# Optimization experiments

Hardware: AMD Instinct MI355X
Metric: run time of the kernel (lower is better)

The kernel has to match this reference:

```python
import jax, jax.numpy as jnp
import numpy as np
import math

D_KEY = 64
D_VALUE = 64
NUM_HEADS = 16
D_MODEL = D_VALUE * NUM_HEADS  # 1024


def setup_inputs() -> dict:
    key = jax.random.key(0)
    ks = jax.random.split(key, 5)
    B, N = 2, 2048
    s = 1.0 / math.sqrt(D_MODEL)
    return {
        "x": jax.random.normal(ks[0], (B, N, D_MODEL), dtype=jnp.float32),
        "Wq": jax.random.normal(ks[1], (D_MODEL, D_KEY * NUM_HEADS), dtype=jnp.float32) * s,
        "Wk": jax.random.normal(ks[2], (D_MODEL, D_KEY * NUM_HEADS), dtype=jnp.float32) * s,
        "Wv": jax.random.normal(ks[3], (D_MODEL, D_MODEL), dtype=jnp.float32) * s,
        "Wp": jax.random.normal(ks[4], (D_MODEL, D_MODEL), dtype=jnp.float32) * s,
    }


def reference(x, Wq, Wk, Wv, Wp):
    # x: [B, N, d_model]. Equivalent to the original block-diagonal concat trick:
    # off-diagonal blocks are -inf, so softmax over the key axis reduces to
    # independent per-head softmax attention.
    B, N, D = x.shape
    H, K, V = NUM_HEADS, D_KEY, D_VALUE
    scale = 1.0 / math.sqrt(K)
    q = (x @ Wq).reshape(B, N, H, K)
    k = (x @ Wk).reshape(B, N, H, K)
    v = (x @ Wv).reshape(B, N, H, V)
    scores = jnp.einsum("bnhk,bmhk->bhnm", q, k) * scale  # [B,H,N,N]
    attn = jax.nn.softmax(scores, axis=-1)
    out = jnp.einsum("bhnm,bmhv->bnhv", attn, v).reshape(B, N, D)
    return x + out @ Wp
```

## Files before the change

kernel.cpp:

```cpp
#include <hip/hip_runtime.h>

typedef float f32x4 __attribute__((ext_vector_type(4)));
typedef __bf16 bf16x8 __attribute__((ext_vector_type(8)));

#define DEV static __device__ __forceinline__

DEV ushort f2bf(float f) {
  unsigned u = __builtin_bit_cast(unsigned, f);
  u += 0x7FFFu + ((u >> 16) & 1u);
  return (ushort)(u >> 16);
}

DEV bf16x8 ld_frag(const ushort* p) {
  return __builtin_bit_cast(bf16x8, *reinterpret_cast<const int4*>(p));
}

DEV bf16x8 ld_lds(const ushort* base, int byte_off) {
  return __builtin_bit_cast(bf16x8,
      *reinterpret_cast<const int4*>(reinterpret_cast<const char*>(base) + byte_off));
}

DEV int swz(int row, int col_byte) { return row * 128 + (col_byte ^ ((row & 7) << 4)); }

DEV float fast_exp2(float x) {
  float r;
  asm("v_exp_f32 %0, %1" : "=v"(r) : "v"(x));
  return r;
}

DEV unsigned cvt_pk_bf16(float lo, float hi) {
  unsigned r;
  asm("v_cvt_pk_bf16_f32 %0, %1, %2" : "=v"(r) : "v"(lo), "v"(hi));
  return r;
}

DEV void gload16(const ushort* g, ushort* l) {
  __builtin_amdgcn_global_load_lds(
      (const __attribute__((address_space(1))) unsigned int*)g,
      (__attribute__((address_space(3))) unsigned int*)l, 16, 0, 0);
}


__global__ __launch_bounds__(256) void convert_x(const float* __restrict__ x,
                                                 ushort* __restrict__ xb) {
  int i = blockIdx.x * 256 + threadIdx.x;
  float4 v = reinterpret_cast<const float4*>(x)[i];
  ushort4 o = make_ushort4(f2bf(v.x), f2bf(v.y), f2bf(v.z), f2bf(v.w));
  reinterpret_cast<ushort4*>(xb)[i] = o;
}

__global__ __launch_bounds__(256) void transpose_w(const float* __restrict__ w0,
                                                   const float* __restrict__ w1,
                                                   const float* __restrict__ w2,
                                                   const float* __restrict__ w3,
                                                   ushort* __restrict__ wt) {
  __shared__ float tile[32][33];
  const int z = blockIdx.z;
  const float* w = z == 0 ? w0 : z == 1 ? w1 : z == 2 ? w2 : w3;
  ushort* out = wt + (size_t)z * 1024 * 1024;
  const int n0 = blockIdx.x * 32, k0 = blockIdx.y * 32;
  const int tx = threadIdx.x, ty = threadIdx.y;
#pragma unroll
  for (int i = 0; i < 4; ++i)
    tile[ty + i * 8][tx] = w[(size_t)(k0 + ty + i * 8) * 1024 + n0 + tx];
  __syncthreads();
#pragma unroll
  for (int i = 0; i < 4; ++i)
    out[(size_t)(n0 + ty + i * 8) * 1024 + k0 + tx] = f2bf(tile[tx][ty + i * 8]);
}


DEV void gemm_core(const ushort* __restrict__ A, const ushort* __restrict__ BT,
                   ushort* a_lds, ushort* b_lds, int row0, int col0, f32x4 acc[4][4]) {
  const int tid = threadIdx.x;
  const int lane = tid & 63;
  const int w = tid >> 6, wr = w >> 1, wc = w & 1;
  const int lg = lane >> 4, l15 = lane & 15;
  const int srow = w * 32 + (lane >> 3);
  const int scol = ((lane & 7) ^ (lane >> 3)) << 3;
  const ushort* ga = A + (size_t)(row0 + srow) * 1024 + scol;
  const ushort* gb = BT + (size_t)(col0 + srow) * 1024 + scol;
#pragma unroll
  for (int ai = 0; ai < 4; ++ai)
#pragma unroll
    for (int bj = 0; bj < 4; ++bj) acc[ai][bj] = f32x4{0.f, 0.f, 0.f, 0.f};

  for (int kt = 0; kt < 1024; kt += 64) {
    __syncthreads();
#pragma unroll
    for (int p = 0; p < 4; ++p) {
      gload16(ga + kt + (size_t)(p * 8) * 1024, a_lds + (w * 32 + p * 8) * 64);
      gload16(gb + kt + (size_t)(p * 8) * 1024, b_lds + (w * 32 + p * 8) * 64);
    }
    __syncthreads();
    bf16x8 af[4][2], bfr[4][2];
#pragma unroll
    for (int i = 0; i < 4; ++i)
#pragma unroll
      for (int kk = 0; kk < 2; ++kk) {
        af[i][kk] = ld_lds(a_lds, swz(wr * 64 + i * 16 + l15, kk * 64 + lg * 16));
        bfr[i][kk] = ld_lds(b_lds, swz(wc * 64 + i * 16 + l15, kk * 64 + lg * 16));
      }
#pragma unroll
    for (int kk = 0; kk < 2; ++kk)
#pragma unroll
      for (int ai = 0; ai < 4; ++ai)
#pragma unroll
        for (int bj = 0; bj < 4; ++bj)
          acc[ai][bj] = __builtin_amdgcn_mfma_f32_16x16x32_bf16(af[ai][kk], bfr[bj][kk],
                                                                acc[ai][bj], 0, 0, 0);
  }
}

__global__ __launch_bounds__(256) void gemm_qkv(const ushort* __restrict__ xb,
                                                const ushort* __restrict__ wqT,
                                                const ushort* __restrict__ wkT,
                                                const ushort* __restrict__ wvT,
                                                ushort* __restrict__ q, ushort* __restrict__ k,
                                                ushort* __restrict__ vt) {
  __shared__ ushort a_lds[128 * 64], b_lds[128 * 64];
  const int fid = blockIdx.x;
  const int wid = (fid & 7) * 96 + (fid >> 3);
  const int row = wid / 24, rem = wid % 24;
  const int col = rem / 3, z = rem % 3;
  const int row0 = row * 128, col0 = col * 128;
  const ushort* BT = z == 0 ? wqT : z == 1 ? wkT : wvT;
  f32x4 acc[4][4];
  gemm_core(xb, BT, a_lds, b_lds, row0, col0, acc);
  const int lane = threadIdx.x & 63;
  const int w = threadIdx.x >> 6, wr = w >> 1, wc = w & 1;
  const int lg = lane >> 4, l15 = lane & 15;
  if (z < 2) {
    ushort* out = z == 0 ? q : k;
    const float sc = z == 0 ? 0.125f * 1.4426950408889634f : 1.0f;
#pragma unroll
    for (int ai = 0; ai < 4; ++ai)
#pragma unroll
      for (int bj = 0; bj < 4; ++bj)
#pragma unroll
        for (int r = 0; r < 4; ++r) {
          int orow = row0 + wr * 64 + ai * 16 + lg * 4 + r;
          int ocol = col0 + wc * 64 + bj * 16 + l15;
          out[(size_t)orow * 1024 + ocol] = f2bf(acc[ai][bj][r] * sc);
        }
  } else {
#pragma unroll
    for (int ai = 0; ai < 4; ++ai)
#pragma unroll
      for (int bj = 0; bj < 4; ++bj) {
        int orow = row0 + wr * 64 + ai * 16 + lg * 4;
        int ocol = col0 + wc * 64 + bj * 16 + l15;
        int bb = orow >> 11, n = orow & 2047;
        ushort4 pk = make_ushort4(f2bf(acc[ai][bj][0]), f2bf(acc[ai][bj][1]),
                                  f2bf(acc[ai][bj][2]), f2bf(acc[ai][bj][3]));
        *reinterpret_cast<ushort4*>(vt + ((size_t)(bb * 1024 + ocol)) * 2048 + n) = pk;
      }
  }
}

__global__ __launch_bounds__(256) void gemm_out(const ushort* __restrict__ ob,
                                                const ushort* __restrict__ wpT,
                                                const float* __restrict__ x,
                                                float* __restrict__ y) {
  __shared__ ushort a_lds[128 * 64], b_lds[64 * 64];
  const int fid = blockIdx.x;
  const int wid = (fid & 7) * 64 + (fid >> 3);
  const int row0 = (wid >> 4) * 128, col0 = (wid & 15) * 64;
  const int tid = threadIdx.x;
  const int lane = tid & 63;
  const int w = tid >> 6, wr = w >> 1, wc = w & 1;
  const int lg = lane >> 4, l15 = lane & 15;
  const int sr8 = lane >> 3;
  const int scol = ((lane & 7) ^ sr8) << 3;
  const ushort* ga = ob + (size_t)(row0 + w * 32 + sr8) * 1024 + scol;
  const ushort* gb = wpT + (size_t)(col0 + w * 16 + sr8) * 1024 + scol;

  f32x4 acc[4][2];
#pragma unroll
  for (int ai = 0; ai < 4; ++ai)
#pragma unroll
    for (int bj = 0; bj < 2; ++bj) acc[ai][bj] = f32x4{0.f, 0.f, 0.f, 0.f};

  for (int kt = 0; kt < 1024; kt += 64) {
    __syncthreads();
#pragma unroll
    for (int p = 0; p < 4; ++p)
      gload16(ga + kt + (size_t)(p * 8) * 1024, a_lds + (w * 32 + p * 8) * 64);
#pragma unroll
    for (int p = 0; p < 2; ++p)
      gload16(gb + kt + (size_t)(p * 8) * 1024, b_lds + (w * 16 + p * 8) * 64);
    __syncthreads();
    bf16x8 af[4][2], bfr[2][2];
#pragma unroll
    for (int kk = 0; kk < 2; ++kk) {
#pragma unroll
      for (int i = 0; i < 4; ++i)
        af[i][kk] = ld_lds(a_lds, swz(wr * 64 + i * 16 + l15, kk * 64 + lg * 16));
#pragma unroll
      for (int j = 0; j < 2; ++j)
        bfr[j][kk] = ld_lds(b_lds, swz(wc * 32 + j * 16 + l15, kk * 64 + lg * 16));
    }
#pragma unroll
    for (int kk = 0; kk < 2; ++kk)
#pragma unroll
      for (int ai = 0; ai < 4; ++ai)
#pragma unroll
        for (int bj = 0; bj < 2; ++bj)
          acc[ai][bj] = __builtin_amdgcn_mfma_f32_16x16x32_bf16(af[ai][kk], bfr[bj][kk],
                                                                acc[ai][bj], 0, 0, 0);
  }

#pragma unroll
  for (int ai = 0; ai < 4; ++ai)
#pragma unroll
    for (int bj = 0; bj < 2; ++bj)
#pragma unroll
      for (int r = 0; r < 4; ++r) {
        int orow = row0 + wr * 64 + ai * 16 + lg * 4 + r;
        int ocol = col0 + wc * 32 + bj * 16 + l15;
        size_t idx = (size_t)orow * 1024 + ocol;
        y[idx] = x[idx] + acc[ai][bj][r];
      }
}

__global__ __launch_bounds__(256) void attn(const ushort* __restrict__ qg,
                                            const ushort* __restrict__ kg,
                                            const ushort* __restrict__ vtg,
                                            ushort* __restrict__ og) {
  __shared__ ushort k_lds[2 * 64 * 64];
  __shared__ ushort v_lds[2 * 64 * 64];
  const int fid = blockIdx.x;
  const int wid = (fid & 7) * 128 + (fid >> 3);
  const int bh = wid >> 5, q0 = wid & 31;
  const int b = bh >> 4, h = bh & 15;
  const int n0 = q0 * 64;
  const int tid = threadIdx.x, lane = tid & 63, w = tid >> 6;
  const int lg = lane >> 4, l15 = lane & 15;

  bf16x8 qf[2];
#pragma unroll
  for (int d32 = 0; d32 < 2; ++d32)
    qf[d32] = ld_frag(qg + (size_t)(b * 2048 + n0 + w * 16 + l15) * 1024 + h * 64 + d32 * 32 + lg * 8);

  f32x4 o[4];
#pragma unroll
  for (int bj = 0; bj < 4; ++bj) o[bj] = f32x4{0.f, 0.f, 0.f, 0.f};
  f32x4 ssum = f32x4{0.f, 0.f, 0.f, 0.f};

  const int sr8 = lane >> 3;
  const int scol = ((lane & 7) ^ sr8) << 3;
  const ushort* kbase = kg + (size_t)(b * 2048 + w * 16 + sr8) * 1024 + h * 64 + scol;
  const ushort* vbase = vtg + (size_t)(b * 1024 + h * 64 + w * 16 + sr8) * 2048 + scol;

  ushort* kB0 = k_lds;
  ushort* kB1 = k_lds + 4096;
  ushort* vB0 = v_lds;
  ushort* vB1 = v_lds + 4096;

  auto stage = [&](ushort* kdst, ushort* vdst, int kv0) {
#pragma unroll
    for (int p = 0; p < 2; ++p) {
      gload16(kbase + (size_t)(kv0 + p * 8) * 1024, kdst + (w * 16 + p * 8) * 64);
      gload16(vbase + (size_t)(p * 8) * 2048 + kv0, vdst + (w * 16 + p * 8) * 64);
    }
  };

  const int4 ones4 = make_int4(0x3F803F80, 0x3F803F80, 0x3F803F80, 0x3F803F80);
  const bf16x8 onesf = __builtin_bit_cast(bf16x8, ones4);

  auto body = [&](const ushort* kb, const ushort* vb) {
    f32x4 s[4];
#pragma unroll
    for (int kj = 0; kj < 4; ++kj) s[kj] = f32x4{0.f, 0.f, 0.f, 0.f};
    __builtin_amdgcn_s_setprio(1);
#pragma unroll
    for (int d32 = 0; d32 < 2; ++d32)
#pragma unroll
      for (int kj = 0; kj < 4; ++kj) {
        bf16x8 kf = ld_lds(kb, swz(kj * 16 + l15, d32 * 64 + lg * 16));
        s[kj] = __builtin_amdgcn_mfma_f32_16x16x32_bf16(kf, qf[d32], s[kj], 0, 0, 0);
      }
    __builtin_amdgcn_s_setprio(0);

    unsigned pk[4][2];
#pragma unroll
    for (int kj = 0; kj < 4; ++kj) {
      float p0 = fast_exp2(s[kj][0]);
      float p1 = fast_exp2(s[kj][1]);
      float p2 = fast_exp2(s[kj][2]);
      float p3 = fast_exp2(s[kj][3]);
      pk[kj][0] = cvt_pk_bf16(p0, p1);
      pk[kj][1] = cvt_pk_bf16(p2, p3);
    }

    bf16x8 pa[2];
#pragma unroll
    for (int k32 = 0; k32 < 2; ++k32) {
      unsigned x0 = pk[2 * k32][0], y0 = pk[2 * k32 + 1][0];
      unsigned x1 = pk[2 * k32][1], y1 = pk[2 * k32 + 1][1];
      asm("v_permlane32_swap_b32 %0, %1" : "+v"(x0), "+v"(y0));
      asm("v_permlane32_swap_b32 %0, %1" : "+v"(x1), "+v"(y1));
      asm("v_permlane16_swap_b32 %0, %1" : "+v"(x0), "+v"(y0));
      asm("v_permlane16_swap_b32 %0, %1" : "+v"(x1), "+v"(y1));
      int4 fr = make_int4(x0, x1, y0, y1);
      pa[k32] = __builtin_bit_cast(bf16x8, fr);
    }

    __builtin_amdgcn_s_setprio(1);
    ssum = __builtin_amdgcn_mfma_f32_16x16x32_bf16(pa[0], onesf, ssum, 0, 0, 0);
    ssum = __builtin_amdgcn_mfma_f32_16x16x32_bf16(pa[1], onesf, ssum, 0, 0, 0);
#pragma unroll
    for (int k32 = 0; k32 < 2; ++k32)
#pragma unroll
      for (int bj = 0; bj < 4; ++bj) {
        bf16x8 vf = ld_lds(vb, swz(bj * 16 + l15, k32 * 64 + lg * 16));
        o[bj] = __builtin_amdgcn_mfma_f32_16x16x32_bf16(pa[k32], vf, o[bj], 0, 0, 0);
      }
    __builtin_amdgcn_s_setprio(0);
  };

  stage(kB0, vB0, 0);
  __syncthreads();

  for (int tt = 0; tt < 16; ++tt) {
    stage(kB1, vB1, (2 * tt + 1) * 64);
    body(kB0, vB0);
    __syncthreads();
    if (tt < 15) stage(kB0, vB0, (2 * tt + 2) * 64);
    body(kB1, vB1);
    __syncthreads();
  }

  f32x4 inv;
#pragma unroll
  for (int r = 0; r < 4; ++r) inv[r] = 1.0f / ssum[r];
#pragma unroll
  for (int bj = 0; bj < 4; ++bj)
#pragma unroll
    for (int r = 0; r < 4; ++r) {
      int n = n0 + w * 16 + lg * 4 + r;
      og[(size_t)(b * 2048 + n) * 1024 + h * 64 + bj * 16 + l15] = f2bf(o[bj][r] * inv[r]);
    }
}


extern "C" void kernel_launch(void* const* d_in, const int* in_sizes, int n_in,
                              void* d_out, int out_size, void* d_ws, size_t ws_size,
                              hipStream_t stream) {
  const float* x = (const float*)d_in[0];
  const float* Wq = (const float*)d_in[1];
  const float* Wk = (const float*)d_in[2];
  const float* Wv = (const float*)d_in[3];
  const float* Wp = (const float*)d_in[4];
  float* y = (float*)d_out;

  char* ws = (char*)d_ws;
  ushort* xb = (ushort*)(ws);
  ushort* wT = (ushort*)(ws + (8ull << 20));
  ushort* qw = (ushort*)(ws + (16ull << 20));
  ushort* kw = (ushort*)(ws + (24ull << 20));
  ushort* vtw = (ushort*)(ws + (32ull << 20));
  ushort* ow = (ushort*)(ws);

  convert_x<<<4096, 256, 0, stream>>>(x, xb);
  transpose_w<<<dim3(32, 32, 4), dim3(32, 8), 0, stream>>>(Wq, Wk, Wv, Wp, wT);
  gemm_qkv<<<768, 256, 0, stream>>>(xb, wT, wT + (1u << 20), wT + (2u << 20), qw, kw, vtw);
  attn<<<1024, 256, 0, stream>>>(qw, kw, vtw, ow);
  gemm_out<<<512, 256, 0, stream>>>(ow, wT + (3u << 20), x, y);
}
```

Before: 120.8 us.

## Double query rows per attention block and process two KV subtiles per stage

```diff
diff --git a/kernel.cpp b/kernel.cpp
--- a/kernel.cpp
+++ b/kernel.cpp
@@ -227,120 +227,148 @@
                                             const ushort* __restrict__ kg,
                                             const ushort* __restrict__ vtg,
                                             ushort* __restrict__ og) {
-  __shared__ ushort k_lds[2 * 64 * 64];
-  __shared__ ushort v_lds[2 * 64 * 64];
+  __shared__ ushort k_lds[4 * 64 * 64];
+  __shared__ ushort v_lds[4 * 64 * 64];
   const int fid = blockIdx.x;
-  const int wid = (fid & 7) * 128 + (fid >> 3);
-  const int bh = wid >> 5, q0 = wid & 31;
+  const int wid = (fid & 7) * 64 + (fid >> 3);
+  const int bh = wid >> 4, q0 = wid & 15;
   const int b = bh >> 4, h = bh & 15;
-  const int n0 = q0 * 64;
+  const int n0 = q0 * 128;
   const int tid = threadIdx.x, lane = tid & 63, w = tid >> 6;
   const int lg = lane >> 4, l15 = lane & 15;
 
-  bf16x8 qf[2];
-#pragma unroll
-  for (int d32 = 0; d32 < 2; ++d32)
-    qf[d32] = ld_frag(qg + (size_t)(b * 2048 + n0 + w * 16 + l15) * 1024 + h * 64 + d32 * 32 + lg * 8);
-
-  f32x4 o[4];
-#pragma unroll
-  for (int bj = 0; bj < 4; ++bj) o[bj] = f32x4{0.f, 0.f, 0.f, 0.f};
-  f32x4 ssum = f32x4{0.f, 0.f, 0.f, 0.f};
+  bf16x8 qf[2][2];
+#pragma unroll
+  for (int qi = 0; qi < 2; ++qi)
+#pragma unroll
+    for (int d32 = 0; d32 < 2; ++d32)
+      qf[qi][d32] = ld_frag(qg + (size_t)(b * 2048 + n0 + w * 32 + qi * 16 + l15) * 1024 +
+                            h * 64 + d32 * 32 + lg * 8);
+
+  f32x4 o[2][4];
+#pragma unroll
+  for (int qi = 0; qi < 2; ++qi)
+#pragma unroll
+    for (int bj = 0; bj < 4; ++bj) o[qi][bj] = f32x4{0.f, 0.f, 0.f, 0.f};
+  f32x4 ssum[2] = {f32x4{0.f, 0.f, 0.f, 0.f}, f32x4{0.f, 0.f, 0.f, 0.f}};
 
   const int sr8 = lane >> 3;
   const int scol = ((lane & 7) ^ sr8) << 3;
   const ushort* kbase = kg + (size_t)(b * 2048 + w * 16 + sr8) * 1024 + h * 64 + scol;
   const ushort* vbase = vtg + (size_t)(b * 1024 + h * 64 + w * 16 + sr8) * 2048 + scol;
 
-  ushort* kB0 = k_lds;
-  ushort* kB1 = k_lds + 4096;
-  ushort* vB0 = v_lds;
-  ushort* vB1 = v_lds + 4096;
-
-  auto stage = [&](ushort* kdst, ushort* vdst, int kv0) {
+  auto stage_sub = [&](ushort* kdst, ushort* vdst, int kv0) {
 #pragma unroll
     for (int p = 0; p < 2; ++p) {
       gload16(kbase + (size_t)(kv0 + p * 8) * 1024, kdst + (w * 16 + p * 8) * 64);
       gload16(vbase + (size_t)(p * 8) * 2048 + kv0, vdst + (w * 16 + p * 8) * 64);
     }
   };
+  auto stage2 = [&](int buf, int kv0) {
+    stage_sub(k_lds + (2 * buf) * 4096, v_lds + (2 * buf) * 4096, kv0);
+    stage_sub(k_lds + (2 * buf + 1) * 4096, v_lds + (2 * buf + 1) * 4096, kv0 + 64);
+  };
 
   const int4 ones4 = make_int4(0x3F803F80, 0x3F803F80, 0x3F803F80, 0x3F803F80);
   const bf16x8 onesf = __builtin_bit_cast(bf16x8, ones4);
 
-  auto body = [&](const ushort* kb, const ushort* vb) {
-    f32x4 s[4];
-#pragma unroll
-    for (int kj = 0; kj < 4; ++kj) s[kj] = f32x4{0.f, 0.f, 0.f, 0.f};
+  auto qk_sub = [&](const ushort* kb, f32x4 s[2][4]) {
+#pragma unroll
+    for (int qi = 0; qi < 2; ++qi)
+#pragma unroll
+      for (int kj = 0; kj < 4; ++kj) s[qi][kj] = f32x4{0.f, 0.f, 0.f, 0.f};
     __builtin_amdgcn_s_setprio(1);
 #pragma unroll
     for (int d32 = 0; d32 < 2; ++d32)
 #pragma unroll
       for (int kj = 0; kj < 4; ++kj) {
         bf16x8 kf = ld_lds(kb, swz(kj * 16 + l15, d32 * 64 + lg * 16));
-        s[kj] = __builtin_amdgcn_mfma_f32_16x16x32_bf16(kf, qf[d32], s[kj], 0, 0, 0);
+        s[0][kj] = __builtin_amdgcn_mfma_f32_16x16x32_bf16(kf, qf[0][d32], s[0][kj], 0, 0, 0);
+        s[1][kj] = __builtin_amdgcn_mfma_f32_16x16x32_bf16(kf, qf[1][d32], s[1][kj], 0, 0, 0);
       }
     __builtin_amdgcn_s_setprio(0);
-
-    unsigned pk[4][2];
-#pragma unroll
-    for (int kj = 0; kj < 4; ++kj) {
-      float p0 = fast_exp2(s[kj][0]);
-      float p1 = fast_exp2(s[kj][1]);
-      float p2 = fast_exp2(s[kj][2]);
-      float p3 = fast_exp2(s[kj][3]);
-      pk[kj][0] = cvt_pk_bf16(p0, p1);
-      pk[kj][1] = cvt_pk_bf16(p2, p3);
-    }
-
-    bf16x8 pa[2];
-#pragma unroll
-    for (int k32 = 0; k32 < 2; ++k32) {
-      unsigned x0 = pk[2 * k32][0], y0 = pk[2 * k32 + 1][0];
-      unsigned x1 = pk[2 * k32][1], y1 = pk[2 * k32 + 1][1];
-      asm("v_permlane32_swap_b32 %0, %1" : "+v"(x0), "+v"(y0));
-      asm("v_permlane32_swap_b32 %0, %1" : "+v"(x1), "+v"(y1));
-      asm("v_permlane16_swap_b32 %0, %1" : "+v"(x0), "+v"(y0));
-      asm("v_permlane16_swap_b32 %0, %1" : "+v"(x1), "+v"(y1));
-      int4 fr = make_int4(x0, x1, y0, y1);
-      pa[k32] = __builtin_bit_cast(bf16x8, fr);
-    }
-
+  };
+
+  auto sm_pv_sub = [&](const ushort* vb, f32x4 s[2][4]) {
+    bf16x8 pa[2][2];
+#pragma unroll
+    for (int qi = 0; qi < 2; ++qi) {
+      unsigned pk[4][2];
+#pragma unroll
+      for (int kj = 0; kj < 4; ++kj) {
+        float p0 = fast_exp2(s[qi][kj][0]);
+        float p1 = fast_exp2(s[qi][kj][1]);
+        float p2 = fast_exp2(s[qi][kj][2]);
+        float p3 = fast_exp2(s[qi][kj][3]);
+        pk[kj][0] = cvt_pk_bf16(p0, p1);
+        pk[kj][1] = cvt_pk_bf16(p2, p3);
+      }
+#pragma unroll
+      for (int k32 = 0; k32 < 2; ++k32) {
+        unsigned x0 = pk[2 * k32][0], y0 = pk[2 * k32 + 1][0];
+        unsigned x1 = pk[2 * k32][1], y1 = pk[2 * k32 + 1][1];
+        asm("v_permlane32_swap_b32 %0, %1" : "+v"(x0), "+v"(y0));
+        asm("v_permlane32_swap_b32 %0, %1" : "+v"(x1), "+v"(y1));
+        asm("v_permlane16_swap_b32 %0, %1" : "+v"(x0), "+v"(y0));
+        asm("v_permlane16_swap_b32 %0, %1" : "+v"(x1), "+v"(y1));
+        int4 fr = make_int4(x0, x1, y0, y1);
+        pa[qi][k32] = __builtin_bit_cast(bf16x8, fr);
+      }
+    }
     __builtin_amdgcn_s_setprio(1);
-    ssum = __builtin_amdgcn_mfma_f32_16x16x32_bf16(pa[0], onesf, ssum, 0, 0, 0);
-    ssum = __builtin_amdgcn_mfma_f32_16x16x32_bf16(pa[1], onesf, ssum, 0, 0, 0);
+#pragma unroll
+    for (int qi = 0; qi < 2; ++qi) {
+      ssum[qi] = __builtin_amdgcn_mfma_f32_16x16x32_bf16(pa[qi][0], onesf, ssum[qi], 0, 0, 0);
+      ssum[qi] = __builtin_amdgcn_mfma_f32_16x16x32_bf16(pa[qi][1], onesf, ssum[qi], 0, 0, 0);
+    }
 #pragma unroll
     for (int k32 = 0; k32 < 2; ++k32)
 #pragma unroll
       for (int bj = 0; bj < 4; ++bj) {
         bf16x8 vf = ld_lds(vb, swz(bj * 16 + l15, k32 * 64 + lg * 16));
-        o[bj] = __builtin_amdgcn_mfma_f32_16x16x32_bf16(pa[k32], vf, o[bj], 0, 0, 0);
+        o[0][bj] = __builtin_amdgcn_mfma_f32_16x16x32_bf16(pa[0][k32], vf, o[0][bj], 0, 0, 0);
+        o[1][bj] = __builtin_amdgcn_mfma_f32_16x16x32_bf16(pa[1][k32], vf, o[1][bj], 0, 0, 0);
       }
     __builtin_amdgcn_s_setprio(0);
   };
 
-  stage(kB0, vB0, 0);
+  auto body2 = [&](int buf) {
+    const ushort* kb0 = k_lds + (2 * buf) * 4096;
+    const ushort* kb1 = k_lds + (2 * buf + 1) * 4096;
+    const ushort* vb0 = v_lds + (2 * buf) * 4096;
+    const ushort* vb1 = v_lds + (2 * buf + 1) * 4096;
+    f32x4 s0[2][4], s1[2][4];
+    qk_sub(kb0, s0);
+    qk_sub(kb1, s1);
+    sm_pv_sub(vb0, s0);
+    sm_pv_sub(vb1, s1);
+  };
+
+  stage2(0, 0);
   __syncthreads();
 
-  for (int tt = 0; tt < 16; ++tt) {
-    stage(kB1, vB1, (2 * tt + 1) * 64);
-    body(kB0, vB0);
-    __syncthreads();
-    if (tt < 15) stage(kB0, vB0, (2 * tt + 2) * 64);
-    body(kB1, vB1);
-    __syncthreads();
-  }
-
-  f32x4 inv;
-#pragma unroll
-  for (int r = 0; r < 4; ++r) inv[r] = 1.0f / ssum[r];
-#pragma unroll
-  for (int bj = 0; bj < 4; ++bj)
-#pragma unroll
-    for (int r = 0; r < 4; ++r) {
-      int n = n0 + w * 16 + lg * 4 + r;
-      og[(size_t)(b * 2048 + n) * 1024 + h * 64 + bj * 16 + l15] = f2bf(o[bj][r] * inv[r]);
-    }
+  for (int tt = 0; tt < 8; ++tt) {
+    stage2(1, (2 * tt + 1) * 128);
+    body2(0);
+    __syncthreads();
+    if (tt < 7) stage2(0, (2 * tt + 2) * 128);
+    body2(1);
+    __syncthreads();
+  }
+
+#pragma unroll
+  for (int qi = 0; qi < 2; ++qi) {
+    f32x4 inv;
+#pragma unroll
+    for (int r = 0; r < 4; ++r) inv[r] = 1.0f / ssum[qi][r];
+#pragma unroll
+    for (int bj = 0; bj < 4; ++bj)
+#pragma unroll
+      for (int r = 0; r < 4; ++r) {
+        int n = n0 + w * 32 + qi * 16 + lg * 4 + r;
+        og[(size_t)(b * 2048 + n) * 1024 + h * 64 + bj * 16 + l15] = f2bf(o[qi][bj][r] * inv[r]);
+      }
+  }
 }
 
 
@@ -365,6 +393,6 @@
   convert_x<<<4096, 256, 0, stream>>>(x, xb);
   transpose_w<<<dim3(32, 32, 4), dim3(32, 8), 0, stream>>>(Wq, Wk, Wv, Wp, wT);
   gemm_qkv<<<768, 256, 0, stream>>>(xb, wT, wT + (1u << 20), wT + (2u << 20), qw, kw, vtw);
-  attn<<<1024, 256, 0, stream>>>(qw, kw, vtw, ow);
+  attn<<<512, 256, 0, stream>>>(qw, kw, vtw, ow);
   gemm_out<<<512, 256, 0, stream>>>(ow, wT + (3u << 20), x, y);
 }
```

Result: faster. 115.0 us (-4.8%).
